# Optimization experiments

Measured on AMD Instinct MI355X. Metric: run time of the kernel, lower is better.

Reference implementation:

```python
import jax, jax.numpy as jnp
import numpy as np

N = 100000   # nodes
E = 1000000  # edges
H = 64       # hidden_channels
METAPATH = (0, 1, 2)


def setup_inputs() -> dict:
    key = jax.random.key(0)
    ks = jax.random.split(key, 32)
    inp = {
        "x": jax.random.normal(ks[0], (N, 2 * H), dtype=jnp.float32),
        "edge_index": jax.random.randint(ks[1], (2, E), 0, N, dtype=jnp.int64),
        "edge_type": jax.random.randint(ks[2], (E,), 0, 3, dtype=jnp.int64),
    }
    # layer 0: in = 2H, layers 1,2: in = H; torch Linear weight is [out, in]
    ki = 3
    for l, in_dim in enumerate([2 * H, H, H]):
        for wname in ["wl", "w0", "w1"]:
            inp[f"{wname}{l}"] = jax.random.normal(ks[ki], (H, in_dim), dtype=jnp.float32) * 0.05
            ki += 1
            inp[f"{wname[0]}b{wname[1]}{l}"] = jnp.zeros((H,), dtype=jnp.float32)
    return inp


def _layer(x_in, h, mask, src, dst, wl, bl, w0, b0, w1, b1):
    # aggr='add', flow='target_to_source': agg[src[e]] += h[dst[e]] for masked edges
    msg = jnp.where(mask[:, None], h[dst], jnp.zeros((), h.dtype))  # [E, H]
    agg = jax.ops.segment_sum(msg, src, num_segments=N)             # [N, H]
    return agg @ wl.T + bl + h @ w0.T + b0 + x_in @ w1.T + b1


def reference(x, edge_index, edge_type,
              wl0, wbl0, w00, wb00, w10, wb10,
              wl1, wbl1, w01, wb01, w11, wb11,
              wl2, wbl2, w02, wb02, w12, wb12):
    src, dst = edge_index[0], edge_index[1]
    params = [
        (wl0, wbl0, w00, wb00, w10, wb10),
        (wl1, wbl1, w01, wb01, w11, wb11),
        (wl2, wbl2, w02, wb02, w12, wb12),
    ]
    h = x
    for i, rel in enumerate(METAPATH):
        mask = edge_type == rel
        x_in = x if i == 0 else h
        h = jax.nn.relu(_layer(x_in, h, mask, src, dst, *params[i]))
        # F.dropout with training=False is identity (eval mode reference)
    return h
```

## Files before the change

### kernel.cpp

```cpp
#include <hip/hip_runtime.h>
#include <cstdint>
#include <cstddef>

#define NNODES 100000
#define NEDGES 1000000
#define NREL 3
#define RN (NREL * NNODES)
#define EPB 2048
#define SCAN_BLOCKS ((RN + EPB - 1) / EPB)
#define LDSTR 68
#define ECAP 768

__device__ __forceinline__ uint32_t pack_bf2(float a, float b) {
    uint32_t ua = __float_as_uint(a), ub = __float_as_uint(b);
    ua = (ua + 0x7fffu + ((ua >> 16) & 1u)) >> 16;
    ub = (ub + 0x7fffu + ((ub >> 16) & 1u)) >> 16;
    return ua | (ub << 16);
}
__device__ __forceinline__ float bf_lo(uint32_t u) { return __uint_as_float(u << 16); }
__device__ __forceinline__ float bf_hi(uint32_t u) { return __uint_as_float(u & 0xffff0000u); }


__global__ __launch_bounds__(256) void hist_kernel(
    const int* __restrict__ srcv, const int* __restrict__ ety, int* __restrict__ cnt)
{
    const int e = (int)(blockIdx.x * 256 + threadIdx.x);
    if (e < NEDGES) atomicAdd(&cnt[ety[e] * NNODES + srcv[e]], 1);
}

__global__ __launch_bounds__(256) void scan_reduce(
    const int* __restrict__ cnt, int* __restrict__ bsum)
{
    __shared__ int sd[256];
    const int t = (int)threadIdx.x;
    const int base = (int)blockIdx.x * EPB + t * 8;
    int s = 0;
    #pragma unroll
    for (int i = 0; i < 8; ++i)
        if (base + i < RN) s += cnt[base + i];
    sd[t] = s;
    __syncthreads();
    for (int st = 128; st > 0; st >>= 1) {
        if (t < st) sd[t] += sd[t + st];
        __syncthreads();
    }
    if (t == 0) bsum[blockIdx.x] = sd[0];
}

__global__ __launch_bounds__(256) void scan_blocksums(int* __restrict__ bsum, int nb)
{
    __shared__ int buf0[256], buf1[256];
    const int t = (int)threadIdx.x;
    buf0[t] = (t < nb) ? bsum[t] : 0;
    __syncthreads();
    int* a = buf0; int* b = buf1;
    for (int st = 1; st < 256; st <<= 1) {
        int v = a[t];
        if (t >= st) v += a[t - st];
        b[t] = v;
        __syncthreads();
        int* tmp = a; a = b; b = tmp;
    }
    if (t < nb) bsum[t] = (t == 0) ? 0 : a[t - 1];
}

__global__ __launch_bounds__(256) void scan_final(
    const int* __restrict__ cnt, const int* __restrict__ bsum,
    int* __restrict__ off, int* __restrict__ wptr)
{
    __shared__ int buf0[256], buf1[256];
    const int t = (int)threadIdx.x;
    const int base = (int)blockIdx.x * EPB + t * 8;
    int v[8];
    int tot = 0;
    #pragma unroll
    for (int i = 0; i < 8; ++i) {
        v[i] = (base + i < RN) ? cnt[base + i] : 0;
        tot += v[i];
    }
    buf0[t] = tot;
    __syncthreads();
    int* a = buf0; int* b = buf1;
    for (int st = 1; st < 256; st <<= 1) {
        int s = a[t];
        if (t >= st) s += a[t - st];
        b[t] = s;
        __syncthreads();
        int* tmp = a; a = b; b = tmp;
    }
    int o = bsum[blockIdx.x] + ((t == 0) ? 0 : a[t - 1]);
    #pragma unroll
    for (int i = 0; i < 8; ++i) {
        if (base + i < RN) { off[base + i] = o; wptr[base + i] = o; }
        o += v[i];
    }
    if (blockIdx.x == 0 && t == 0) off[RN] = NEDGES;
}

__global__ __launch_bounds__(256) void fill_kernel(
    const int* __restrict__ srcv, const int* __restrict__ dstv,
    const int* __restrict__ ety, int* __restrict__ wptr, int* __restrict__ ebuf)
{
    const int e = (int)(blockIdx.x * 256 + threadIdx.x);
    if (e < NEDGES) {
        const int pos = atomicAdd(&wptr[ety[e] * NNODES + srcv[e]], 1);
        ebuf[pos] = dstv[e];
    }
}

template<int K>
__global__ __launch_bounds__(256) void gemm_y(
    const float* __restrict__ A, const float* __restrict__ W,
    uint32_t* __restrict__ y, int nNodes)
{
    __shared__ float As[16 * LDSTR];
    __shared__ float Ws[16 * LDSTR];

    const int t  = (int)threadIdx.x;
    const int tx = t & 15, ty = t >> 4;
    const int n0 = (int)blockIdx.x * 64;
    const int srow = t >> 2, skk = (t & 3) * 4;
    const int nA = n0 + srow;

    float4 acc[4];
    #pragma unroll
    for (int i = 0; i < 4; ++i) acc[i] = make_float4(0.f, 0.f, 0.f, 0.f);

    #pragma unroll 1
    for (int c = 0; c < K / 16; ++c) {
        const int k0 = c * 16;
        float4 av = make_float4(0.f, 0.f, 0.f, 0.f);
        if (nA < nNodes) av = *(const float4*)(A + (size_t)nA * K + k0 + skk);
        const float4 wv4 = *(const float4*)(W + (size_t)srow * K + k0 + skk);

        __syncthreads();
        As[(skk + 0) * LDSTR + srow] = av.x; As[(skk + 1) * LDSTR + srow] = av.y;
        As[(skk + 2) * LDSTR + srow] = av.z; As[(skk + 3) * LDSTR + srow] = av.w;
        Ws[(skk + 0) * LDSTR + srow] = wv4.x; Ws[(skk + 1) * LDSTR + srow] = wv4.y;
        Ws[(skk + 2) * LDSTR + srow] = wv4.z; Ws[(skk + 3) * LDSTR + srow] = wv4.w;
        __syncthreads();

        #pragma unroll
        for (int k = 0; k < 16; ++k) {
            const float4 a4 = *(const float4*)&As[k * LDSTR + ty * 4];
            const float4 w4 = *(const float4*)&Ws[k * LDSTR + tx * 4];
            acc[0].x = fmaf(a4.x, w4.x, acc[0].x); acc[0].y = fmaf(a4.x, w4.y, acc[0].y);
            acc[0].z = fmaf(a4.x, w4.z, acc[0].z); acc[0].w = fmaf(a4.x, w4.w, acc[0].w);
            acc[1].x = fmaf(a4.y, w4.x, acc[1].x); acc[1].y = fmaf(a4.y, w4.y, acc[1].y);
            acc[1].z = fmaf(a4.y, w4.z, acc[1].z); acc[1].w = fmaf(a4.y, w4.w, acc[1].w);
            acc[2].x = fmaf(a4.z, w4.x, acc[2].x); acc[2].y = fmaf(a4.z, w4.y, acc[2].y);
            acc[2].z = fmaf(a4.z, w4.z, acc[2].z); acc[2].w = fmaf(a4.z, w4.w, acc[2].w);
            acc[3].x = fmaf(a4.w, w4.x, acc[3].x); acc[3].y = fmaf(a4.w, w4.y, acc[3].y);
            acc[3].z = fmaf(a4.w, w4.z, acc[3].z); acc[3].w = fmaf(a4.w, w4.w, acc[3].w);
        }
    }

    #pragma unroll
    for (int i = 0; i < 4; ++i) {
        const int n = n0 + ty * 4 + i;
        if (n < nNodes) {
            uint2 p;
            p.x = pack_bf2(acc[i].x, acc[i].y);
            p.y = pack_bf2(acc[i].z, acc[i].w);
            *(uint2*)(y + (size_t)n * 32 + tx * 2) = p;
        }
    }
}

template<int K, bool HASY>
__global__ __launch_bounds__(256) void dense_layer(
    const float* __restrict__ h,
    const uint32_t* __restrict__ ybuf,
    const int* __restrict__ off, const int* __restrict__ ebuf, int rel,
    const float* __restrict__ W2a, const float* __restrict__ W2b,
    const float* __restrict__ B1, const float* __restrict__ B2, const float* __restrict__ B3,
    const float* __restrict__ Wy,
    float* __restrict__ out,
    uint32_t* __restrict__ ynext,
    int nNodes)
{
    __shared__ float As[16 * LDSTR];
    __shared__ float Ws[16 * LDSTR];
    __shared__ uint32_t Ot[HASY ? 64 : 1][36];
    __shared__ int Eids[ECAP];

    const int t  = (int)threadIdx.x;
    const int tx = t & 15, ty = t >> 4;
    const int n0 = (int)blockIdx.x * 64;
    const int srow = t >> 2, skk = (t & 3) * 4;
    const int nA = n0 + srow;

    const int* o = off + rel * NNODES;
    const int nend = (n0 + 64 < nNodes) ? n0 + 64 : nNodes;
    const int s0 = o[n0];
    const int blkLen = o[nend] - s0;
    for (int i = t; i < blkLen && i < ECAP; i += 256) Eids[i] = ebuf[s0 + i];

    int jj[4], ee[4];
    #pragma unroll
    for (int i = 0; i < 4; ++i) {
        const int n = n0 + ty * 4 + i;
        if (n < nNodes) { jj[i] = o[n]; ee[i] = o[n + 1]; }
        else            { jj[i] = 0;    ee[i] = 0; }
    }

    float4 acc[4];
    #pragma unroll
    for (int i = 0; i < 4; ++i) acc[i] = make_float4(0.f, 0.f, 0.f, 0.f);

    #pragma unroll 1
    for (int c = 0; c < K / 16; ++c) {
        const int k0 = c * 16;
        float4 av = make_float4(0.f, 0.f, 0.f, 0.f);
        if (nA < nNodes) av = *(const float4*)(h + (size_t)nA * K + k0 + skk);
        const float4 a = *(const float4*)(W2a + (size_t)srow * K + k0 + skk);
        const float4 b = *(const float4*)(W2b + (size_t)srow * K + k0 + skk);
        const float4 wv4 = make_float4(a.x + b.x, a.y + b.y, a.z + b.z, a.w + b.w);

        __syncthreads();
        As[(skk + 0) * LDSTR + srow] = av.x; As[(skk + 1) * LDSTR + srow] = av.y;
        As[(skk + 2) * LDSTR + srow] = av.z; As[(skk + 3) * LDSTR + srow] = av.w;
        Ws[(skk + 0) * LDSTR + srow] = wv4.x; Ws[(skk + 1) * LDSTR + srow] = wv4.y;
        Ws[(skk + 2) * LDSTR + srow] = wv4.z; Ws[(skk + 3) * LDSTR + srow] = wv4.w;
        __syncthreads();

        #pragma unroll
        for (int k = 0; k < 16; ++k) {
            const float4 a4 = *(const float4*)&As[k * LDSTR + ty * 4];
            const float4 w4 = *(const float4*)&Ws[k * LDSTR + tx * 4];
            acc[0].x = fmaf(a4.x, w4.x, acc[0].x); acc[0].y = fmaf(a4.x, w4.y, acc[0].y);
            acc[0].z = fmaf(a4.x, w4.z, acc[0].z); acc[0].w = fmaf(a4.x, w4.w, acc[0].w);
            acc[1].x = fmaf(a4.y, w4.x, acc[1].x); acc[1].y = fmaf(a4.y, w4.y, acc[1].y);
            acc[1].z = fmaf(a4.y, w4.z, acc[1].z); acc[1].w = fmaf(a4.y, w4.w, acc[1].w);
            acc[2].x = fmaf(a4.z, w4.x, acc[2].x); acc[2].y = fmaf(a4.z, w4.y, acc[2].y);
            acc[2].z = fmaf(a4.z, w4.z, acc[2].z); acc[2].w = fmaf(a4.z, w4.w, acc[2].w);
            acc[3].x = fmaf(a4.w, w4.x, acc[3].x); acc[3].y = fmaf(a4.w, w4.y, acc[3].y);
            acc[3].z = fmaf(a4.w, w4.z, acc[3].z); acc[3].w = fmaf(a4.w, w4.w, acc[3].w);
        }
    }

    float4 g[4];
    #pragma unroll
    for (int i = 0; i < 4; ++i) g[i] = make_float4(0.f, 0.f, 0.f, 0.f);

    for (;;) {
        int d[4];
        bool any = false;
        #pragma unroll
        for (int i = 0; i < 4; ++i) {
            d[i] = -1;
            if (jj[i] < ee[i]) {
                const int idx = jj[i] - s0;
                d[i] = (idx < ECAP) ? Eids[idx] : ebuf[jj[i]];
                any = true;
            }
        }
        if (!any) break;
        uint2 v[4];
        #pragma unroll
        for (int i = 0; i < 4; ++i) {
            v[i] = make_uint2(0u, 0u);
            if (d[i] >= 0) v[i] = *(const uint2*)(ybuf + (size_t)d[i] * 32 + tx * 2);
        }
        #pragma unroll
        for (int i = 0; i < 4; ++i) {
            if (d[i] >= 0) {
                g[i].x += bf_lo(v[i].x); g[i].y += bf_hi(v[i].x);
                g[i].z += bf_lo(v[i].y); g[i].w += bf_hi(v[i].y);
                jj[i]++;
            }
        }
    }

    const float4 b1 = *(const float4*)(B1 + tx * 4);
    const float4 b2 = *(const float4*)(B2 + tx * 4);
    const float4 b3 = *(const float4*)(B3 + tx * 4);
    const float4 bias = make_float4(b1.x + b2.x + b3.x, b1.y + b2.y + b3.y,
                                    b1.z + b2.z + b3.z, b1.w + b2.w + b3.w);
    #pragma unroll
    for (int i = 0; i < 4; ++i) {
        const int n = n0 + ty * 4 + i;
        float4 r = make_float4(acc[i].x + bias.x + g[i].x, acc[i].y + bias.y + g[i].y,
                               acc[i].z + bias.z + g[i].z, acc[i].w + bias.w + g[i].w);
        r.x = r.x > 0.f ? r.x : 0.f;
        r.y = r.y > 0.f ? r.y : 0.f;
        r.z = r.z > 0.f ? r.z : 0.f;
        r.w = r.w > 0.f ? r.w : 0.f;
        if (n < nNodes) *(float4*)(out + (size_t)n * 64 + tx * 4) = r;
        if constexpr (HASY) {
            uint2 p;
            p.x = pack_bf2(r.x, r.y);
            p.y = pack_bf2(r.z, r.w);
            *(uint2*)&Ot[ty * 4 + i][tx * 2] = p;
        }
    }

    if constexpr (HASY) {
        float4 ya[4];
        #pragma unroll
        for (int i = 0; i < 4; ++i) ya[i] = make_float4(0.f, 0.f, 0.f, 0.f);

        #pragma unroll 1
        for (int c = 0; c < 4; ++c) {
            const float4 wv4 = *(const float4*)(Wy + (size_t)srow * 64 + c * 16 + skk);
            __syncthreads();
            Ws[(skk + 0) * LDSTR + srow] = wv4.x; Ws[(skk + 1) * LDSTR + srow] = wv4.y;
            Ws[(skk + 2) * LDSTR + srow] = wv4.z; Ws[(skk + 3) * LDSTR + srow] = wv4.w;
            __syncthreads();
            #pragma unroll
            for (int k4 = 0; k4 < 4; ++k4) {
                const float4 w0 = *(const float4*)&Ws[(k4 * 4 + 0) * LDSTR + tx * 4];
                const float4 w1 = *(const float4*)&Ws[(k4 * 4 + 1) * LDSTR + tx * 4];
                const float4 w2 = *(const float4*)&Ws[(k4 * 4 + 2) * LDSTR + tx * 4];
                const float4 w3 = *(const float4*)&Ws[(k4 * 4 + 3) * LDSTR + tx * 4];
                #pragma unroll
                for (int i = 0; i < 4; ++i) {
                    const uint2 u = *(const uint2*)&Ot[ty * 4 + i][c * 8 + k4 * 2];
                    const float4 a4 = make_float4(bf_lo(u.x), bf_hi(u.x), bf_lo(u.y), bf_hi(u.y));
                    ya[i].x = fmaf(a4.x, w0.x, ya[i].x); ya[i].y = fmaf(a4.x, w0.y, ya[i].y);
                    ya[i].z = fmaf(a4.x, w0.z, ya[i].z); ya[i].w = fmaf(a4.x, w0.w, ya[i].w);
                    ya[i].x = fmaf(a4.y, w1.x, ya[i].x); ya[i].y = fmaf(a4.y, w1.y, ya[i].y);
                    ya[i].z = fmaf(a4.y, w1.z, ya[i].z); ya[i].w = fmaf(a4.y, w1.w, ya[i].w);
                    ya[i].x = fmaf(a4.z, w2.x, ya[i].x); ya[i].y = fmaf(a4.z, w2.y, ya[i].y);
                    ya[i].z = fmaf(a4.z, w2.z, ya[i].z); ya[i].w = fmaf(a4.z, w2.w, ya[i].w);
                    ya[i].x = fmaf(a4.w, w3.x, ya[i].x); ya[i].y = fmaf(a4.w, w3.y, ya[i].y);
                    ya[i].z = fmaf(a4.w, w3.z, ya[i].z); ya[i].w = fmaf(a4.w, w3.w, ya[i].w);
                }
            }
        }
        #pragma unroll
        for (int i = 0; i < 4; ++i) {
            const int n = n0 + ty * 4 + i;
            if (n < nNodes) {
                uint2 p;
                p.x = pack_bf2(ya[i].x, ya[i].y);
                p.y = pack_bf2(ya[i].z, ya[i].w);
                *(uint2*)(ynext + (size_t)n * 32 + tx * 2) = p;
            }
        }
    }
}

extern "C" void kernel_launch(void* const* d_in, const int* in_sizes, int n_in,
                              void* d_out, int out_size, void* d_ws, size_t ws_size,
                              hipStream_t stream)
{
    const float* x    = (const float*)d_in[0];
    const int*   eidx = (const int*)d_in[1];
    const int*   ety  = (const int*)d_in[2];
    const int*   srcv = eidx;
    const int*   dstv = eidx + NEDGES;

    const float* wl0 = (const float*)d_in[3];
    const float* bl0 = (const float*)d_in[4];
    const float* w00 = (const float*)d_in[5];
    const float* b00 = (const float*)d_in[6];
    const float* w10 = (const float*)d_in[7];
    const float* b10 = (const float*)d_in[8];

    const float* wl1 = (const float*)d_in[9];
    const float* bl1 = (const float*)d_in[10];
    const float* w01 = (const float*)d_in[11];
    const float* b01 = (const float*)d_in[12];
    const float* w11 = (const float*)d_in[13];
    const float* b11 = (const float*)d_in[14];

    const float* wl2 = (const float*)d_in[15];
    const float* bl2 = (const float*)d_in[16];
    const float* w02 = (const float*)d_in[17];
    const float* b02 = (const float*)d_in[18];
    const float* w12 = (const float*)d_in[19];
    const float* b12 = (const float*)d_in[20];

    char* p = (char*)d_ws;
    auto alloc = [&](size_t bytes) {
        char* r = p;
        p += (bytes + 255) & ~(size_t)255;
        return r;
    };
    int* cnt  = (int*)alloc((size_t)RN * 4);
    int* off  = (int*)alloc((size_t)(RN + 1) * 4);
    int* wptr = (int*)alloc((size_t)RN * 4);
    int* bsum = (int*)alloc(1024);
    int* ebuf = (int*)alloc((size_t)NEDGES * 4);
    uint32_t* yA = (uint32_t*)alloc((size_t)NNODES * 32 * 4);
    uint32_t* yB = (uint32_t*)alloc((size_t)NNODES * 32 * 4);
    float* h2    = (float*)alloc((size_t)NNODES * 64 * sizeof(float));
    float* h1    = (float*)d_out;

    const int edgeGrid  = (NEDGES + 255) / 256;
    const int tileGrid  = (NNODES + 63) / 64;

    hipMemsetAsync(cnt, 0, (size_t)RN * 4, stream);
    hist_kernel<<<edgeGrid, 256, 0, stream>>>(srcv, ety, cnt);
    scan_reduce<<<SCAN_BLOCKS, 256, 0, stream>>>(cnt, bsum);
    scan_blocksums<<<1, 256, 0, stream>>>(bsum, SCAN_BLOCKS);
    scan_final<<<SCAN_BLOCKS, 256, 0, stream>>>(cnt, bsum, off, wptr);
    fill_kernel<<<edgeGrid, 256, 0, stream>>>(srcv, dstv, ety, wptr, ebuf);

    gemm_y<128><<<tileGrid, 256, 0, stream>>>(x, wl0, yA, NNODES);

    dense_layer<128, true><<<tileGrid, 256, 0, stream>>>(
        x, yA, off, ebuf, 0, w00, w10, bl0, b00, b10, wl1, h1, yB, NNODES);

    dense_layer<64, true><<<tileGrid, 256, 0, stream>>>(
        h1, yB, off, ebuf, 1, w01, w11, bl1, b01, b11, wl2, h2, yA, NNODES);

    dense_layer<64, false><<<tileGrid, 256, 0, stream>>>(
        h2, yA, off, ebuf, 2, w02, w12, bl2, b02, b12, nullptr,
        (float*)d_out, nullptr, NNODES);
}
```

Baseline: 436.2 us.

## Interleave neighbor gather with GEMM k-chunks and drop LDS edge-id staging

The CSR neighbor gather of bf16 rows is now interleaved with the FMA inner loop, issuing one gather step per half k-chunk so its global-load latency overlaps the dense matmul. Edge ids are prefetched one ahead per row from global memory instead of being staged in a shared-memory buffer, which removes that LDS array and its fill loop. The cost is more live registers, and the edge-id reads become dependent global loads.

```diff
diff --git a/kernel.cpp b/kernel.cpp
--- a/kernel.cpp
+++ b/kernel.cpp
@@ -9,7 +9,6 @@
 #define EPB 2048
 #define SCAN_BLOCKS ((RN + EPB - 1) / EPB)
 #define LDSTR 68
-#define ECAP 768
 
 __device__ __forceinline__ uint32_t pack_bf2(float a, float b) {
     uint32_t ua = __float_as_uint(a), ub = __float_as_uint(b);
@@ -182,7 +181,6 @@
     __shared__ float As[16 * LDSTR];
     __shared__ float Ws[16 * LDSTR];
     __shared__ uint32_t Ot[HASY ? 64 : 1][36];
-    __shared__ int Eids[ECAP];
 
     const int t  = (int)threadIdx.x;
     const int tx = t & 15, ty = t >> 4;
@@ -191,41 +189,50 @@
     const int nA = n0 + srow;
 
     const int* o = off + rel * NNODES;
-    const int nend = (n0 + 64 < nNodes) ? n0 + 64 : nNodes;
-    const int s0 = o[n0];
-    const int blkLen = o[nend] - s0;
-    for (int i = t; i < blkLen && i < ECAP; i += 256) Eids[i] = ebuf[s0 + i];
-
-    int jj[4], ee[4];
+    int jj[4], ee[4], dd[4];
     #pragma unroll
     for (int i = 0; i < 4; ++i) {
         const int n = n0 + ty * 4 + i;
         if (n < nNodes) { jj[i] = o[n]; ee[i] = o[n + 1]; }
         else            { jj[i] = 0;    ee[i] = 0; }
     }
-
-    float4 acc[4];
-    #pragma unroll
-    for (int i = 0; i < 4; ++i) acc[i] = make_float4(0.f, 0.f, 0.f, 0.f);
-
-    #pragma unroll 1
-    for (int c = 0; c < K / 16; ++c) {
-        const int k0 = c * 16;
-        float4 av = make_float4(0.f, 0.f, 0.f, 0.f);
-        if (nA < nNodes) av = *(const float4*)(h + (size_t)nA * K + k0 + skk);
-        const float4 a = *(const float4*)(W2a + (size_t)srow * K + k0 + skk);
-        const float4 b = *(const float4*)(W2b + (size_t)srow * K + k0 + skk);
-        const float4 wv4 = make_float4(a.x + b.x, a.y + b.y, a.z + b.z, a.w + b.w);
-
-        __syncthreads();
-        As[(skk + 0) * LDSTR + srow] = av.x; As[(skk + 1) * LDSTR + srow] = av.y;
-        As[(skk + 2) * LDSTR + srow] = av.z; As[(skk + 3) * LDSTR + srow] = av.w;
-        Ws[(skk + 0) * LDSTR + srow] = wv4.x; Ws[(skk + 1) * LDSTR + srow] = wv4.y;
-        Ws[(skk + 2) * LDSTR + srow] = wv4.z; Ws[(skk + 3) * LDSTR + srow] = wv4.w;
-        __syncthreads();
-
-        #pragma unroll
-        for (int k = 0; k < 16; ++k) {
+    #pragma unroll
+    for (int i = 0; i < 4; ++i)
+        dd[i] = (jj[i] < ee[i]) ? ebuf[jj[i]] : -1;
+
+    float4 acc[4], g[4];
+    #pragma unroll
+    for (int i = 0; i < 4; ++i) {
+        acc[i] = make_float4(0.f, 0.f, 0.f, 0.f);
+        g[i]   = make_float4(0.f, 0.f, 0.f, 0.f);
+    }
+    uint2 vv[4];
+    int nd[4];
+
+    auto gather_issue = [&]() {
+        #pragma unroll
+        for (int i = 0; i < 4; ++i) {
+            vv[i] = make_uint2(0u, 0u);
+            nd[i] = -1;
+            if (dd[i] >= 0) {
+                vv[i] = *(const uint2*)(ybuf + (size_t)dd[i] * 32 + tx * 2);
+                if (jj[i] + 1 < ee[i]) nd[i] = ebuf[jj[i] + 1];
+            }
+        }
+    };
+    auto gather_acc = [&]() {
+        #pragma unroll
+        for (int i = 0; i < 4; ++i) {
+            if (dd[i] >= 0) {
+                g[i].x += bf_lo(vv[i].x); g[i].y += bf_hi(vv[i].x);
+                g[i].z += bf_lo(vv[i].y); g[i].w += bf_hi(vv[i].y);
+                jj[i]++; dd[i] = nd[i];
+            }
+        }
+    };
+    auto fma_half = [&](int kbeg) {
+        #pragma unroll
+        for (int k = kbeg; k < kbeg + 8; ++k) {
             const float4 a4 = *(const float4*)&As[k * LDSTR + ty * 4];
             const float4 w4 = *(const float4*)&Ws[k * LDSTR + tx * 4];
             acc[0].x = fmaf(a4.x, w4.x, acc[0].x); acc[0].y = fmaf(a4.x, w4.y, acc[0].y);
@@ -237,39 +244,36 @@
             acc[3].x = fmaf(a4.w, w4.x, acc[3].x); acc[3].y = fmaf(a4.w, w4.y, acc[3].y);
             acc[3].z = fmaf(a4.w, w4.z, acc[3].z); acc[3].w = fmaf(a4.w, w4.w, acc[3].w);
         }
-    }
-
-    float4 g[4];
-    #pragma unroll
-    for (int i = 0; i < 4; ++i) g[i] = make_float4(0.f, 0.f, 0.f, 0.f);
+    };
+
+    #pragma unroll 1
+    for (int c = 0; c < K / 16; ++c) {
+        const int k0 = c * 16;
+        float4 av = make_float4(0.f, 0.f, 0.f, 0.f);
+        if (nA < nNodes) av = *(const float4*)(h + (size_t)nA * K + k0 + skk);
+        const float4 a = *(const float4*)(W2a + (size_t)srow * K + k0 + skk);
+        const float4 b = *(const float4*)(W2b + (size_t)srow * K + k0 + skk);
+        const float4 wv4 = make_float4(a.x + b.x, a.y + b.y, a.z + b.z, a.w + b.w);
+
+        __syncthreads();
+        As[(skk + 0) * LDSTR + srow] = av.x; As[(skk + 1) * LDSTR + srow] = av.y;
+        As[(skk + 2) * LDSTR + srow] = av.z; As[(skk + 3) * LDSTR + srow] = av.w;
+        Ws[(skk + 0) * LDSTR + srow] = wv4.x; Ws[(skk + 1) * LDSTR + srow] = wv4.y;
+        Ws[(skk + 2) * LDSTR + srow] = wv4.z; Ws[(skk + 3) * LDSTR + srow] = wv4.w;
+        __syncthreads();
+
+        gather_issue();
+        fma_half(0);
+        gather_acc();
+        gather_issue();
+        fma_half(8);
+        gather_acc();
+    }
 
     for (;;) {
-        int d[4];
-        bool any = false;
-        #pragma unroll
-        for (int i = 0; i < 4; ++i) {
-            d[i] = -1;
-            if (jj[i] < ee[i]) {
-                const int idx = jj[i] - s0;
-                d[i] = (idx < ECAP) ? Eids[idx] : ebuf[jj[i]];
-                any = true;
-            }
-        }
-        if (!any) break;
-        uint2 v[4];
-        #pragma unroll
-        for (int i = 0; i < 4; ++i) {
-            v[i] = make_uint2(0u, 0u);
-            if (d[i] >= 0) v[i] = *(const uint2*)(ybuf + (size_t)d[i] * 32 + tx * 2);
-        }
-        #pragma unroll
-        for (int i = 0; i < 4; ++i) {
-            if (d[i] >= 0) {
-                g[i].x += bf_lo(v[i].x); g[i].y += bf_hi(v[i].x);
-                g[i].z += bf_lo(v[i].y); g[i].w += bf_hi(v[i].y);
-                jj[i]++;
-            }
-        }
+        if (dd[0] < 0 && dd[1] < 0 && dd[2] < 0 && dd[3] < 0) break;
+        gather_issue();
+        gather_acc();
     }
 
     const float4 b1 = *(const float4*)(B1 + tx * 4);
```

Measured after the change: 452.4 us. +3.7%, slower.
